# Optimization experiments

Hardware: AMD Instinct MI355X
Metric: run time of the kernel (lower is better)

Reference implementation:

```python
import jax, jax.numpy as jnp
import numpy as np

HEAD_DIM = 64
NUM_LANDMARKS = 64
SEQ_LEN = 4096
N_ITER = 6


def setup_inputs() -> dict:
    key = jax.random.key(0)
    kq, kk, kv = jax.random.split(key, 3)
    shape = (4, 12, SEQ_LEN, HEAD_DIM)  # [B, H, S, D]
    return {
        "Q": jax.random.normal(kq, shape, dtype=jnp.float32),
        "K": jax.random.normal(kk, shape, dtype=jnp.float32),
        "V": jax.random.normal(kv, shape, dtype=jnp.float32),
    }


def iterative_inv(mat, n_iter=N_ITER):
    # Newton-Schulz iteration for Moore-Penrose pseudo-inverse.
    L = mat.shape[-1]
    I = jnp.eye(L, dtype=mat.dtype)
    Km = mat
    # global (over all batch/head) max of row/col L1 norms
    scale = 1.0 / (jnp.max(jnp.sum(jnp.abs(Km), axis=-2)) * jnp.max(jnp.sum(jnp.abs(Km), axis=-1)))
    Vm = scale * jnp.swapaxes(Km, -1, -2)
    for _ in range(n_iter):
        KV = jnp.matmul(Km, Vm)
        Vm = jnp.matmul(0.25 * Vm, 13.0 * I - jnp.matmul(KV, 15.0 * I - jnp.matmul(KV, 7.0 * I - KV)))
    return Vm


def reference(Q, K, V):
    B, H, S, D = Q.shape
    m = NUM_LANDMARKS
    inv_scale = 1.0 / np.sqrt(np.sqrt(HEAD_DIM))
    Q = Q * inv_scale
    K = K * inv_scale
    # landmark pooling: mean over segments of length S // m
    Q_land = Q.reshape(B, H, m, S // m, D).mean(axis=-2)  # [B,H,m,D]
    K_land = K.reshape(B, H, m, S // m, D).mean(axis=-2)  # [B,H,m,D]
    kernel_1 = jax.nn.softmax(jnp.einsum("bhsd,bhmd->bhsm", Q, K_land), axis=-1)      # [B,H,S,m]
    kernel_2 = jax.nn.softmax(jnp.einsum("bhmd,bhnd->bhmn", Q_land, K_land), axis=-1)  # [B,H,m,m]
    kernel_3 = jax.nn.softmax(jnp.einsum("bhmd,bhsd->bhms", Q_land, K), axis=-1)       # [B,H,m,S]
    X = jnp.matmul(jnp.matmul(kernel_1, iterative_inv(kernel_2)), jnp.matmul(kernel_3, V))
    return X
```

## Files before the change

kernel.cpp:

```cpp
#include <hip/hip_runtime.h>
#include <cstdint>

#define BH 48
#define SEQ 4096
#define DIM 64
#define SEG 64
#define NCHUNK 8
#define CHUNK 512
#define PAD 68
#define BSTR 72

static constexpr float INV_SCALE = 0.35355339059327379f;

#define OFF_QL   0u
#define OFF_KL   196608u
#define OFF_K2   393216u
#define OFF_W    589824u
#define OFF_P    786432u
#define OFF_MNUM 983040u
#define OFF_MDEN 2555904u
#define OFF_CMAX 2580480u
#define OFF_RMAX 2580528u

typedef __attribute__((ext_vector_type(8))) short short8;
typedef __attribute__((ext_vector_type(4))) float f32x4;
#define MFMA16(a,b,c) __builtin_amdgcn_mfma_f32_16x16x32_bf16(a,b,c,0,0,0)

__device__ __forceinline__ float4 ld4(const float* p){ return *reinterpret_cast<const float4*>(p); }
__device__ __forceinline__ void st4(float* p, float4 v){ *reinterpret_cast<float4*>(p) = v; }

__device__ __forceinline__ unsigned short bfh_(float x){
  unsigned u = __float_as_uint(x);
  return (unsigned short)((u + 0x7fffu + ((u>>16)&1u)) >> 16);
}
__device__ __forceinline__ unsigned short bfl_(float x, unsigned short h){
  float r = x - __uint_as_float(((unsigned)h)<<16);
  return (unsigned short)(__float_as_uint(r) >> 16);
}
__device__ __forceinline__ void split4(float4 v, uint2& hi, uint2& lo){
  unsigned short h0=bfh_(v.x), h1=bfh_(v.y), h2=bfh_(v.z), h3=bfh_(v.w);
  unsigned short l0=bfl_(v.x,h0), l1=bfl_(v.y,h1), l2=bfl_(v.z,h2), l3=bfl_(v.w,h3);
  hi = make_uint2((unsigned)h0 | ((unsigned)h1<<16), (unsigned)h2 | ((unsigned)h3<<16));
  lo = make_uint2((unsigned)l0 | ((unsigned)l1<<16), (unsigned)l2 | ((unsigned)l3<<16));
}
__device__ __forceinline__ short8 mk8(uint2 a, uint2 b){
  union { short8 s; uint4 u; } x; x.u = make_uint4(a.x,a.y,b.x,b.y); return x.s;
}

__device__ __forceinline__ void mm_tile(float c[4][4], const float (*A)[PAD], const float (*B)[PAD], int i0, int j0){
  #pragma unroll 4
  for(int k=0;k<64;k+=4){
    float4 a4[4];
    #pragma unroll
    for(int r=0;r<4;r++) a4[r] = ld4(&A[i0+r][k]);
    #pragma unroll
    for(int kk=0;kk<4;kk++){
      float4 bv = ld4(&B[k+kk][j0]);
      #pragma unroll
      for(int r=0;r<4;r++){
        float a = ((const float*)&a4[r])[kk];
        c[r][0] += a*bv.x; c[r][1] += a*bv.y; c[r][2] += a*bv.z; c[r][3] += a*bv.w;
      }
    }
  }
}

__device__ __forceinline__ void mm_tile_gA(float c[4][4], const float* __restrict__ gA, const float (*B)[PAD], int i0, int j0){
  #pragma unroll 4
  for(int k=0;k<64;k+=4){
    float4 a4[4];
    #pragma unroll
    for(int r=0;r<4;r++) a4[r] = ld4(gA + (i0+r)*64 + k);
    #pragma unroll
    for(int kk=0;kk<4;kk++){
      float4 bv = ld4(&B[k+kk][j0]);
      #pragma unroll
      for(int r=0;r<4;r++){
        float a = ((const float*)&a4[r])[kk];
        c[r][0] += a*bv.x; c[r][1] += a*bv.y; c[r][2] += a*bv.z; c[r][3] += a*bv.w;
      }
    }
  }
}

__device__ __forceinline__ void mm_tile_diag(float c[4][4], const float (*A)[PAD], const float (*B)[PAD], int i0, int j0, float dg){
  #pragma unroll 4
  for(int k=0;k<64;k+=4){
    float4 a4[4];
    #pragma unroll
    for(int r=0;r<4;r++) a4[r] = ld4(&A[i0+r][k]);
    #pragma unroll
    for(int kk=0;kk<4;kk++){
      float4 bv = ld4(&B[k+kk][j0]);
      float b0=-bv.x, b1=-bv.y, b2=-bv.z, b3=-bv.w;
      int dd = k+kk-j0;
      if(dd==0) b0+=dg; else if(dd==1) b1+=dg; else if(dd==2) b2+=dg; else if(dd==3) b3+=dg;
      #pragma unroll
      for(int r=0;r<4;r++){
        float a = ((const float*)&a4[r])[kk];
        c[r][0]+=a*b0; c[r][1]+=a*b1; c[r][2]+=a*b2; c[r][3]+=a*b3;
      }
    }
  }
}

__global__ __launch_bounds__(256) void pool_kernel(const float* __restrict__ Qg, const float* __restrict__ Kg, float* __restrict__ ws){
  int bx = blockIdx.x;
  int head = bx >> 5;
  int rest = bx & 31;
  int tensor = rest >> 4;
  int l0 = (rest & 15) * 4;
  int t = threadIdx.x;
  int ll = t >> 6;
  int lane = t & 63;
  int d4 = (lane & 15) * 4;
  int rq = lane >> 4;
  const float* src = tensor ? Kg : Qg;
  float* dst = ws + (tensor ? OFF_KL : OFF_QL);
  int l = l0 + ll;
  const float* base = src + ((size_t)head*SEQ + (size_t)l*SEG)*DIM + d4;
  float sx=0.f, sy=0.f, sz=0.f, sw=0.f;
  #pragma unroll 4
  for(int r=rq; r<SEG; r+=4){
    float4 v = ld4(base + (size_t)r*DIM);
    sx+=v.x; sy+=v.y; sz+=v.z; sw+=v.w;
  }
  sx += __shfl_xor(sx,16); sy += __shfl_xor(sy,16); sz += __shfl_xor(sz,16); sw += __shfl_xor(sw,16);
  sx += __shfl_xor(sx,32); sy += __shfl_xor(sy,32); sz += __shfl_xor(sz,32); sw += __shfl_xor(sw,32);
  if(rq==0){
    const float sc = INV_SCALE / 64.0f;
    float4 o; o.x=sx*sc; o.y=sy*sc; o.z=sz*sc; o.w=sw*sc;
    st4(dst + ((size_t)head*64 + l)*DIM + d4, o);
  }
}

__global__ __launch_bounds__(256) void k2_kernel(float* __restrict__ ws){
  __shared__ float sQ[64][65];
  __shared__ float sK[64][65];
  __shared__ float sE[64][65];
  __shared__ float red[128];
  int h = blockIdx.x, t = threadIdx.x;
  const float* QL = ws + OFF_QL + (size_t)h*4096;
  const float* KL = ws + OFF_KL + (size_t)h*4096;
  for(int i=t;i<4096;i+=256){ sQ[i>>6][i&63]=QL[i]; sK[i>>6][i&63]=KL[i]; }
  __syncthreads();
  int i = t>>2, q = t&3;
  float l[16];
  #pragma unroll
  for(int jj=0;jj<16;jj++){
    int j = q*16+jj;
    float s=0.f;
    for(int d=0;d<64;d++) s += sQ[i][d]*sK[j][d];
    l[jj]=s;
  }
  float mx = l[0];
  #pragma unroll
  for(int jj=1;jj<16;jj++) mx = fmaxf(mx,l[jj]);
  mx = fmaxf(mx, __shfl_xor(mx,1));
  mx = fmaxf(mx, __shfl_xor(mx,2));
  float sum=0.f;
  #pragma unroll
  for(int jj=0;jj<16;jj++){ l[jj]=__expf(l[jj]-mx); sum+=l[jj]; }
  sum += __shfl_xor(sum,1);
  sum += __shfl_xor(sum,2);
  float inv = 1.0f/sum;
  #pragma unroll
  for(int jj=0;jj<16;jj++) sE[i][q*16+jj] = l[jj]*inv;
  __syncthreads();
  float* K2 = ws + OFF_K2 + (size_t)h*4096;
  for(int idx=t; idx<4096; idx+=256) K2[idx] = sE[idx>>6][idx&63];
  if(t<64){
    float cs=0.f, rs=0.f;
    for(int r=0;r<64;r++){ cs += sE[r][t]; rs += sE[t][r]; }
    red[t]=cs; red[64+t]=rs;
  }
  __syncthreads();
  if(t==0){
    float cm=0.f, rm=0.f;
    for(int j=0;j<64;j++){ cm=fmaxf(cm,red[j]); rm=fmaxf(rm,red[64+j]); }
    ws[OFF_CMAX+h]=cm; ws[OFF_RMAX+h]=rm;
  }
}

__global__ __launch_bounds__(256) void fused_kernel(const float* __restrict__ Kg, const float* __restrict__ Vg, float* __restrict__ ws){
  __shared__ __align__(16) unsigned char smem[74752];
  __shared__ float sscale;
  int bid = blockIdx.x, t = threadIdx.x;
  const int lane=t&63, w=t>>6, ln=lane&15, g=lane>>4;
  const int rr=t>>4, c4=(t&15)*4;
  if(bid < BH){
    int h = bid;
    const float* K2 = ws + OFF_K2 + (size_t)h*4096;
    unsigned short* Uh=(unsigned short*)smem;
    unsigned short* Ul=Uh+4608;
    unsigned short* Rh=Uh+9216;
    unsigned short* Rl=Uh+13824;
    unsigned short* Ch=Uh+18432;
    unsigned short* Cl=Uh+23040;
    unsigned short* Gh=Uh+27648;
    unsigned short* Gl=Uh+32256;
    short8 kmh[2],kml[2];
    #pragma unroll
    for(int kh=0;kh<2;kh++){
      const float* p=K2+(16*w+ln)*64+32*kh+8*g;
      float4 x0=ld4(p), x1=ld4(p+4);
      uint2 h0,l0,h1,l1; split4(x0,h0,l0); split4(x1,h1,l1);
      kmh[kh]=mk8(h0,h1); kml[kh]=mk8(l0,l1);
    }
    if(t<64){
      float cm=(lane<BH)?ws[OFF_CMAX+lane]:0.f;
      float rm=(lane<BH)?ws[OFF_RMAX+lane]:0.f;
      #pragma unroll
      for(int s=32;s>=1;s>>=1){ cm=fmaxf(cm,__shfl_xor(cm,s)); rm=fmaxf(rm,__shfl_xor(rm,s)); }
      if(t==0) sscale=1.0f/(cm*rm);
    }
    __syncthreads();
    float scale=sscale;
    #pragma unroll
    for(int gg=0;gg<4;gg++){
      int m=rr+16*gg;
      float4 v=ld4(K2+m*64+c4);
      v.x*=scale; v.y*=scale; v.z*=scale; v.w*=scale;
      uint2 hi,lo; split4(v,hi,lo);
      *reinterpret_cast<uint2*>(Uh+m*BSTR+c4)=hi;
      *reinterpret_cast<uint2*>(Ul+m*BSTR+c4)=lo;
      float fv[4]={v.x,v.y,v.z,v.w};
      #pragma unroll
      for(int e=0;e<4;e++){
        unsigned short hv=bfh_(fv[e]);
        Rh[(c4+e)*BSTR+m]=hv;
        Rl[(c4+e)*BSTR+m]=bfl_(fv[e],hv);
      }
    }
    __syncthreads();
    f32x4 dA[4];
    short8 ah[2],al[2];
    for(int it=0; it<5; it++){
      #pragma unroll
      for(int ni=0;ni<4;ni++){
        f32x4 d=(f32x4){0.f,0.f,0.f,0.f};
        #pragma unroll
        for(int kh=0;kh<2;kh++){
          int bb=(16*ni+ln)*BSTR+32*kh+8*g;
          short8 bh=*reinterpret_cast<const short8*>(Uh+bb);
          short8 bl=*reinterpret_cast<const short8*>(Ul+bb);
          d=MFMA16(kmh[kh],bh,d); d=MFMA16(kmh[kh],bl,d); d=MFMA16(kml[kh],bh,d);
        }
        dA[ni]=d;
      }
      #pragma unroll
      for(int ni=0;ni<4;ni++){
        int j=16*ni+ln;
        float4 tv; float* pv=(float*)&tv;
        #pragma unroll
        for(int r=0;r<4;r++){
          float v=dA[ni][r];
          int i=16*w+4*g+r;
          unsigned short hv=bfh_(v);
          Ch[i*BSTR+j]=hv; Cl[i*BSTR+j]=bfl_(v,hv);
          pv[r]=((i==j)?7.0f:0.0f)-v;
        }
        uint2 hi,lo; split4(tv,hi,lo);
        *reinterpret_cast<uint2*>(Gh+j*BSTR+16*w+4*g)=hi;
        *reinterpret_cast<uint2*>(Gl+j*BSTR+16*w+4*g)=lo;
      }
      __syncthreads();
      #pragma unroll
      for(int kh=0;kh<2;kh++){
        int ab=(16*w+ln)*BSTR+32*kh+8*g;
        ah[kh]=*reinterpret_cast<const short8*>(Ch+ab);
        al[kh]=*reinterpret_cast<const short8*>(Cl+ab);
      }
      #pragma unroll
      for(int ni=0;ni<4;ni++){
        f32x4 d=(f32x4){0.f,0.f,0.f,0.f};
        #pragma unroll
        for(int kh=0;kh<2;kh++){
          int bb=(16*ni+ln)*BSTR+32*kh+8*g;
          short8 bh=*reinterpret_cast<const short8*>(Gh+bb);
          short8 bl=*reinterpret_cast<const short8*>(Gl+bb);
          d=MFMA16(ah[kh],bh,d); d=MFMA16(ah[kh],bl,d); d=MFMA16(al[kh],bh,d);
        }
        dA[ni]=d;
      }
      __syncthreads();
      #pragma unroll
      for(int ni=0;ni<4;ni++){
        int j=16*ni+ln;
        float4 tv; float* pv=(float*)&tv;
        #pragma unroll
        for(int r=0;r<4;r++){ int i=16*w+4*g+r; pv[r]=((i==j)?15.0f:0.0f)-dA[ni][r]; }
        uint2 hi,lo; split4(tv,hi,lo);
        *reinterpret_cast<uint2*>(Gh+j*BSTR+16*w+4*g)=hi;
        *reinterpret_cast<uint2*>(Gl+j*BSTR+16*w+4*g)=lo;
      }
      __syncthreads();
      #pragma unroll
      for(int ni=0;ni<4;ni++){
        f32x4 d=(f32x4){0.f,0.f,0.f,0.f};
        #pragma unroll
        for(int kh=0;kh<2;kh++){
          int bb=(16*ni+ln)*BSTR+32*kh+8*g;
          short8 bh=*reinterpret_cast<const short8*>(Gh+bb);
          short8 bl=*reinterpret_cast<const short8*>(Gl+bb);
          d=MFMA16(ah[kh],bh,d); d=MFMA16(ah[kh],bl,d); d=MFMA16(al[kh],bh,d);
        }
        dA[ni]=d;
      }
      __syncthreads();
      #pragma unroll
      for(int ni=0;ni<4;ni++){
        int j=16*ni+ln;
        float4 tv; float* pv=(float*)&tv;
        #pragma unroll
        for(int r=0;r<4;r++){ int i=16*w+4*g+r; pv[r]=((i==j)?13.0f:0.0f)-dA[ni][r]; }
        uint2 hi,lo; split4(tv,hi,lo);
        *reinterpret_cast<uint2*>(Ch+j*BSTR+16*w+4*g)=hi;
        *reinterpret_cast<uint2*>(Cl+j*BSTR+16*w+4*g)=lo;
      }
      __syncthreads();
      #pragma unroll
      for(int kh=0;kh<2;kh++){
        int ab=(16*w+ln)*BSTR+32*kh+8*g;
        ah[kh]=*reinterpret_cast<const short8*>(Rh+ab);
        al[kh]=*reinterpret_cast<const short8*>(Rl+ab);
      }
      #pragma unroll
      for(int ni=0;ni<4;ni++){
        f32x4 d=(f32x4){0.f,0.f,0.f,0.f};
        #pragma unroll
        for(int kh=0;kh<2;kh++){
          int bb=(16*ni+ln)*BSTR+32*kh+8*g;
          short8 bh=*reinterpret_cast<const short8*>(Ch+bb);
          short8 bl=*reinterpret_cast<const short8*>(Cl+bb);
          d=MFMA16(ah[kh],bh,d); d=MFMA16(ah[kh],bl,d); d=MFMA16(al[kh],bh,d);
        }
        dA[ni]=d;
      }
      __syncthreads();
      #pragma unroll
      for(int ni=0;ni<4;ni++){
        int j=16*ni+ln;
        float4 tv; float* pv=(float*)&tv;
        #pragma unroll
        for(int r=0;r<4;r++){
          float v=0.25f*dA[ni][r];
          int i=16*w+4*g+r;
          unsigned short hv=bfh_(v);
          Rh[i*BSTR+j]=hv; Rl[i*BSTR+j]=bfl_(v,hv);
          pv[r]=v;
        }
        uint2 hi,lo; split4(tv,hi,lo);
        *reinterpret_cast<uint2*>(Uh+j*BSTR+16*w+4*g)=hi;
        *reinterpret_cast<uint2*>(Ul+j*BSTR+16*w+4*g)=lo;
      }
      __syncthreads();
    }
    float (*Vmf)[PAD]=(float(*)[PAD])(smem+36864);
    for(int i=t;i<4096;i+=256){
      int r_=i>>6, c_=i&63;
      float v=__uint_as_float(((unsigned)Rh[r_*BSTR+c_])<<16)
             +__uint_as_float(((unsigned)Rl[r_*BSTR+c_])<<16);
      Vmf[r_][c_]=v;
    }
    __syncthreads();
    float (*B1)[PAD]=(float(*)[PAD])(smem);
    float (*B2)[PAD]=(float(*)[PAD])(smem+17408);
    int i0=(t>>4)*4, j0=(t&15)*4;
    {
      float c[4][4]={};
      mm_tile_gA(c,K2,Vmf,i0,j0);
      #pragma unroll
      for(int r=0;r<4;r++){ float4 o; o.x=c[r][0];o.y=c[r][1];o.z=c[r][2];o.w=c[r][3]; st4(&B1[i0+r][j0],o); }
      __syncthreads();
    }
    {
      float c[4][4]={};
      mm_tile_diag(c,B1,B1,i0,j0,7.0f);
      #pragma unroll
      for(int r=0;r<4;r++){ float4 o; o.x=c[r][0];o.y=c[r][1];o.z=c[r][2];o.w=c[r][3]; st4(&B2[i0+r][j0],o); }
      __syncthreads();
    }
    {
      float c[4][4]={};
      mm_tile_diag(c,B1,B2,i0,j0,15.0f);
      __syncthreads();
      #pragma unroll
      for(int r=0;r<4;r++){ float4 o; o.x=c[r][0];o.y=c[r][1];o.z=c[r][2];o.w=c[r][3]; st4(&B1[i0+r][j0],o); }
      __syncthreads();
    }
    {
      float c[4][4]={};
      mm_tile_diag(c,Vmf,B1,i0,j0,13.0f);
      __syncthreads();
      #pragma unroll
      for(int r=0;r<4;r++){ float4 o; o.x=0.25f*c[r][0];o.y=0.25f*c[r][1];o.z=0.25f*c[r][2];o.w=0.25f*c[r][3]; st4(&Vmf[i0+r][j0],o); }
      __syncthreads();
    }
    float* W = ws + OFF_W + (size_t)h*4096;
    for(int i=t;i<4096;i+=256) W[i] = Vmf[i>>6][i&63];
  } else {
    int b = bid - BH;
    int h = b >> 3, ch = b & 7;
    unsigned short* QLh=(unsigned short*)smem;
    unsigned short* QLl=QLh+4608;
    unsigned short* Kth=QLh+9216;
    unsigned short* Ktl=QLh+13824;
    unsigned short* VTh=QLh+18432;
    unsigned short* VTl=QLh+23040;
    unsigned short* PTh=QLh+27648;
    unsigned short* PTl=QLh+32256;
    float* sden=(float*)(smem+73728);
    const float* QL = ws + OFF_QL + (size_t)h*4096;
    #pragma unroll
    for(int gg=0;gg<4;gg++){
      int m=rr+16*gg;
      float4 v=ld4(QL+m*64+c4);
      uint2 hi,lo; split4(v,hi,lo);
      *reinterpret_cast<uint2*>(QLh+m*BSTR+c4)=hi;
      *reinterpret_cast<uint2*>(QLl+m*BSTR+c4)=lo;
    }
    const size_t kbase=((size_t)h*SEQ+(size_t)ch*CHUNK)*DIM;
    float4 kr[4],vr[4];
    #pragma unroll
    for(int gg=0;gg<4;gg++){
      size_t off=kbase+(size_t)(rr+16*gg)*DIM+c4;
      kr[gg]=ld4(Kg+off); vr[gg]=ld4(Vg+off);
    }
    f32x4 acc[4];
    #pragma unroll
    for(int ni=0;ni<4;ni++) acc[ni]=(f32x4){0.f,0.f,0.f,0.f};
    float den_acc[4]={0.f,0.f,0.f,0.f};
    for(int tile=0;tile<8;tile++){
      __syncthreads();
      #pragma unroll
      for(int gg=0;gg<4;gg++){
        int r=rr+16*gg;
        float4 kv=kr[gg];
        kv.x*=INV_SCALE; kv.y*=INV_SCALE; kv.z*=INV_SCALE; kv.w*=INV_SCALE;
        uint2 hi,lo; split4(kv,hi,lo);
        *reinterpret_cast<uint2*>(Kth+r*BSTR+c4)=hi;
        *reinterpret_cast<uint2*>(Ktl+r*BSTR+c4)=lo;
        float fv[4]={vr[gg].x,vr[gg].y,vr[gg].z,vr[gg].w};
        #pragma unroll
        for(int e=0;e<4;e++){
          int d=c4+e;
          unsigned short hv=bfh_(fv[e]);
          unsigned short lv=bfl_(fv[e],hv);
          int sp = r ^ (((d>>2)&7)<<3);
          VTh[d*BSTR+sp]=hv; VTl[d*BSTR+sp]=lv;
        }
      }
      if(tile<7){
        #pragma unroll
        for(int gg=0;gg<4;gg++){
          size_t off=kbase+(size_t)((tile+1)*64+rr+16*gg)*DIM+c4;
          kr[gg]=ld4(Kg+off); vr[gg]=ld4(Vg+off);
        }
      }
      __syncthreads();
      short8 kah[2],kal[2];
      #pragma unroll
      for(int kh=0;kh<2;kh++){
        int ab=(16*w+ln)*BSTR+32*kh+8*g;
        kah[kh]=*reinterpret_cast<const short8*>(Kth+ab);
        kal[kh]=*reinterpret_cast<const short8*>(Ktl+ab);
      }
      #pragma unroll
      for(int ni=0;ni<4;ni++){
        f32x4 dl=(f32x4){0.f,0.f,0.f,0.f};
        #pragma unroll
        for(int kh=0;kh<2;kh++){
          int bb=(16*ni+ln)*BSTR+32*kh+8*g;
          short8 bh=*reinterpret_cast<const short8*>(QLh+bb);
          short8 bl=*reinterpret_cast<const short8*>(QLl+bb);
          dl=MFMA16(kah[kh],bh,dl);
          dl=MFMA16(kah[kh],bl,dl);
          dl=MFMA16(kal[kh],bh,dl);
        }
        float p0=__expf(dl[0]), p1=__expf(dl[1]), p2=__expf(dl[2]), p3=__expf(dl[3]);
        den_acc[ni]+=p0+p1+p2+p3;
        unsigned short h0=bfh_(p0),h1=bfh_(p1),h2=bfh_(p2),h3=bfh_(p3);
        unsigned short l0=bfl_(p0,h0),l1=bfl_(p1,h1),l2=bfl_(p2,h2),l3=bfl_(p3,h3);
        int pb=(16*ni+ln)*BSTR+16*w+4*g;
        *reinterpret_cast<uint2*>(PTh+pb)=make_uint2((unsigned)h0|((unsigned)h1<<16),(unsigned)h2|((unsigned)h3<<16));
        *reinterpret_cast<uint2*>(PTl+pb)=make_uint2((unsigned)l0|((unsigned)l1<<16),(unsigned)l2|((unsigned)l3<<16));
      }
      __syncthreads();
      short8 pah[2],pal[2];
      #pragma unroll
      for(int kh=0;kh<2;kh++){
        int pb=(16*w+ln)*BSTR+32*kh+8*g;
        pah[kh]=*reinterpret_cast<const short8*>(PTh+pb);
        pal[kh]=*reinterpret_cast<const short8*>(PTl+pb);
      }
      #pragma unroll
      for(int ni=0;ni<4;ni++){
        int row=16*ni+ln;
        int swz=((row>>2)&7)<<3;
        #pragma unroll
        for(int kh=0;kh<2;kh++){
          int vb=row*BSTR+((32*kh+8*g)^swz);
          short8 vh=*reinterpret_cast<const short8*>(VTh+vb);
          short8 vl=*reinterpret_cast<const short8*>(VTl+vb);
          acc[ni]=MFMA16(pah[kh],vh,acc[ni]);
          acc[ni]=MFMA16(pah[kh],vl,acc[ni]);
          acc[ni]=MFMA16(pal[kh],vh,acc[ni]);
        }
      }
    }
    float* num = ws + OFF_MNUM + (size_t)b*4096;
    #pragma unroll
    for(int ni=0;ni<4;ni++){
      #pragma unroll
      for(int r=0;r<4;r++) num[(16*w+4*g+r)*64+16*ni+ln]=acc[ni][r];
      den_acc[ni]+=__shfl_xor(den_acc[ni],16);
      den_acc[ni]+=__shfl_xor(den_acc[ni],32);
    }
    if(lane<16){
      #pragma unroll
      for(int ni=0;ni<4;ni++) sden[w*64+16*ni+lane]=den_acc[ni];
    }
    __syncthreads();
    if(t<64) ws[OFF_MDEN+(size_t)b*64+t]=sden[t]+sden[64+t]+sden[128+t]+sden[192+t];
  }
}

__global__ __launch_bounds__(256) void combine_kernel(float* __restrict__ ws){
  __shared__ float sW[64][PAD];
  __shared__ float sM[64][PAD];
  __shared__ float sden[64];
  int h=blockIdx.x, t=threadIdx.x;
  if(t<64){
    float s=0.f;
    for(int c=0;c<NCHUNK;c++) s += ws[OFF_MDEN + ((size_t)h*NCHUNK+c)*64 + t];
    sden[t]=1.0f/s;
  }
  for(int i=t;i<4096;i+=256) sW[i>>6][i&63] = ws[OFF_W + (size_t)h*4096 + i];
  __syncthreads();
  for(int i=t;i<1024;i+=256){
    int m=i>>4, d4=(i&15)*4;
    float sx=0.f,sy=0.f,sz=0.f,sw2=0.f;
    for(int c=0;c<NCHUNK;c++){
      float4 v = ld4(ws + OFF_MNUM + ((size_t)h*NCHUNK+c)*4096 + m*64 + d4);
      sx+=v.x; sy+=v.y; sz+=v.z; sw2+=v.w;
    }
    float iv = sden[m];
    float4 o; o.x=sx*iv; o.y=sy*iv; o.z=sz*iv; o.w=sw2*iv;
    st4(&sM[m][d4], o);
  }
  __syncthreads();
  int i0=(t>>4)*4, j0=(t&15)*4;
  float c[4][4]={};
  mm_tile(c, sW, sM, i0, j0);
  float* P = ws + OFF_P + (size_t)h*4096;
  #pragma unroll
  for(int r=0;r<4;r++){
    float4 o; o.x=c[r][0]; o.y=c[r][1]; o.z=c[r][2]; o.w=c[r][3];
    st4(P + (i0+r)*64 + j0, o);
  }
}

__global__ __launch_bounds__(256) void final_kernel(const float* __restrict__ Qg, float* __restrict__ out, const float* __restrict__ ws){
  __shared__ float sKLT[64][PAD];
  __shared__ float sP[64][PAD];
  __shared__ float sQE[64][PAD];
  int bid=blockIdx.x, t=threadIdx.x;
  int h=bid>>6, s0=(bid&63)*64;
  const float* KL = ws + OFF_KL + (size_t)h*4096;
  const float* P  = ws + OFF_P  + (size_t)h*4096;
  const float* Qb = Qg + ((size_t)h*SEQ + (size_t)s0)*DIM;
  for(int i=t;i<1024;i+=256){
    int m=i>>4, d4=(i&15)*4;
    float4 v = ld4(KL + m*64 + d4);
    sKLT[d4+0][m]=v.x; sKLT[d4+1][m]=v.y; sKLT[d4+2][m]=v.z; sKLT[d4+3][m]=v.w;
    st4(&sP[m][d4], ld4(P + m*64 + d4));
    float4 q = ld4(Qb + (size_t)m*DIM + d4);
    q.x*=INV_SCALE; q.y*=INV_SCALE; q.z*=INV_SCALE; q.w*=INV_SCALE;
    st4(&sQE[m][d4], q);
  }
  __syncthreads();
  int i0=(t>>4)*4, j0=(t&15)*4;
  float l[4][4]={};
  mm_tile(l, sQE, sKLT, i0, j0);
  float e[4][4]; float rs[4];
  #pragma unroll
  for(int r=0;r<4;r++){
    float s=0.f;
    #pragma unroll
    for(int cc=0;cc<4;cc++){ e[r][cc]=__expf(l[r][cc]); s+=e[r][cc]; }
    rs[r]=s;
  }
  #pragma unroll
  for(int r=0;r<4;r++){
    rs[r]+=__shfl_xor(rs[r],1);
    rs[r]+=__shfl_xor(rs[r],2);
    rs[r]+=__shfl_xor(rs[r],4);
    rs[r]+=__shfl_xor(rs[r],8);
  }
  __syncthreads();
  #pragma unroll
  for(int r=0;r<4;r++){ float4 o; o.x=e[r][0]; o.y=e[r][1]; o.z=e[r][2]; o.w=e[r][3]; st4(&sQE[i0+r][j0], o); }
  __syncthreads();
  float c[4][4]={};
  mm_tile(c, sQE, sP, i0, j0);
  #pragma unroll
  for(int r=0;r<4;r++){
    float iv = 1.0f/rs[r];
    float4 o; o.x=c[r][0]*iv; o.y=c[r][1]*iv; o.z=c[r][2]*iv; o.w=c[r][3]*iv;
    st4(out + ((size_t)h*SEQ + (size_t)(s0+i0+r))*DIM + j0, o);
  }
}

extern "C" void kernel_launch(void* const* d_in, const int* in_sizes, int n_in,
                              void* d_out, int out_size, void* d_ws, size_t ws_size,
                              hipStream_t stream) {
  const float* Q = (const float*)d_in[0];
  const float* K = (const float*)d_in[1];
  const float* V = (const float*)d_in[2];
  float* out = (float*)d_out;
  float* ws  = (float*)d_ws;

  pool_kernel   <<<BH*32, 256, 0, stream>>>(Q, K, ws);
  k2_kernel     <<<BH,    256, 0, stream>>>(ws);
  fused_kernel  <<<BH + BH*NCHUNK, 256, 0, stream>>>(K, V, ws);
  combine_kernel<<<BH,    256, 0, stream>>>(ws);
  final_kernel  <<<BH*64, 256, 0, stream>>>(Q, out, ws);
}
```

Baseline: 269.7 us.

## Use split-bf16 MFMA for final landmark softmax and P matmuls

Rewrites final_kernel so both 64x64x64 products (Q·K_land^T and softmax·P) run on bf16 MFMA instructions, using a hi/lo split with three MFMAs to keep near-fp32 accuracy, in place of scalar FP32 register tiling. Operands are staged in LDS as bf16 hi/lo planes, and the buffers are reused for the transposed P and the exp tile. Row sums are reduced through shuffles plus a small LDS array. This trades extra packing work and a precision risk from the bf16x3 approximation for higher matrix throughput. Output stores become scalar rather than float4, which may reduce store coalescing.

```diff
diff --git a/kernel.cpp b/kernel.cpp
--- a/kernel.cpp
+++ b/kernel.cpp
@@ -562,53 +562,110 @@
 }
 
 __global__ __launch_bounds__(256) void final_kernel(const float* __restrict__ Qg, float* __restrict__ out, const float* __restrict__ ws){
-  __shared__ float sKLT[64][PAD];
-  __shared__ float sP[64][PAD];
-  __shared__ float sQE[64][PAD];
+  __shared__ __align__(16) unsigned char smem[37888];
   int bid=blockIdx.x, t=threadIdx.x;
   int h=bid>>6, s0=(bid&63)*64;
+  const int lane=t&63, w=t>>6, ln=lane&15, g=lane>>4;
+  const int rr=t>>4, c4=(t&15)*4;
+  unsigned short* QBh=(unsigned short*)smem;
+  unsigned short* QBl=QBh+4608;
+  unsigned short* KLh=QBh+9216;
+  unsigned short* KLl=QBh+13824;
+  float* sdenw=(float*)(smem+36864);
   const float* KL = ws + OFF_KL + (size_t)h*4096;
   const float* P  = ws + OFF_P  + (size_t)h*4096;
   const float* Qb = Qg + ((size_t)h*SEQ + (size_t)s0)*DIM;
-  for(int i=t;i<1024;i+=256){
-    int m=i>>4, d4=(i&15)*4;
-    float4 v = ld4(KL + m*64 + d4);
-    sKLT[d4+0][m]=v.x; sKLT[d4+1][m]=v.y; sKLT[d4+2][m]=v.z; sKLT[d4+3][m]=v.w;
-    st4(&sP[m][d4], ld4(P + m*64 + d4));
-    float4 q = ld4(Qb + (size_t)m*DIM + d4);
+  float4 p2r[4];
+  #pragma unroll
+  for(int gg=0;gg<4;gg++){
+    int row=rr+16*gg;
+    p2r[gg]=ld4(P+row*64+c4);
+    float4 q=ld4(Qb+(size_t)row*DIM+c4);
     q.x*=INV_SCALE; q.y*=INV_SCALE; q.z*=INV_SCALE; q.w*=INV_SCALE;
-    st4(&sQE[m][d4], q);
-  }
-  __syncthreads();
-  int i0=(t>>4)*4, j0=(t&15)*4;
-  float l[4][4]={};
-  mm_tile(l, sQE, sKLT, i0, j0);
-  float e[4][4]; float rs[4];
+    uint2 hi,lo; split4(q,hi,lo);
+    *reinterpret_cast<uint2*>(QBh+row*BSTR+c4)=hi;
+    *reinterpret_cast<uint2*>(QBl+row*BSTR+c4)=lo;
+    float4 kl=ld4(KL+row*64+c4);
+    split4(kl,hi,lo);
+    *reinterpret_cast<uint2*>(KLh+row*BSTR+c4)=hi;
+    *reinterpret_cast<uint2*>(KLl+row*BSTR+c4)=lo;
+  }
+  __syncthreads();
+  short8 ah_[2],al_[2];
+  #pragma unroll
+  for(int kh=0;kh<2;kh++){
+    int ab=(16*w+ln)*BSTR+32*kh+8*g;
+    ah_[kh]=*reinterpret_cast<const short8*>(KLh+ab);
+    al_[kh]=*reinterpret_cast<const short8*>(KLl+ab);
+  }
+  f32x4 dl[4];
+  #pragma unroll
+  for(int ni=0;ni<4;ni++){
+    f32x4 d=(f32x4){0.f,0.f,0.f,0.f};
+    #pragma unroll
+    for(int kh=0;kh<2;kh++){
+      int bb=(16*ni+ln)*BSTR+32*kh+8*g;
+      short8 bh=*reinterpret_cast<const short8*>(QBh+bb);
+      short8 bl=*reinterpret_cast<const short8*>(QBl+bb);
+      d=MFMA16(ah_[kh],bh,d); d=MFMA16(ah_[kh],bl,d); d=MFMA16(al_[kh],bh,d);
+    }
+    dl[ni]=d;
+  }
+  __syncthreads();
+  #pragma unroll
+  for(int gg=0;gg<4;gg++){
+    int row=rr+16*gg;
+    float fp[4]={p2r[gg].x,p2r[gg].y,p2r[gg].z,p2r[gg].w};
+    #pragma unroll
+    for(int e=0;e<4;e++){
+      unsigned short hv=bfh_(fp[e]);
+      QBh[(c4+e)*BSTR+row]=hv;
+      QBl[(c4+e)*BSTR+row]=bfl_(fp[e],hv);
+    }
+  }
+  float den_acc[4];
+  #pragma unroll
+  for(int ni=0;ni<4;ni++){
+    float p0=__expf(dl[ni][0]), p1=__expf(dl[ni][1]), p2v=__expf(dl[ni][2]), p3v=__expf(dl[ni][3]);
+    den_acc[ni]=p0+p1+p2v+p3v;
+    unsigned short h0=bfh_(p0),h1=bfh_(p1),h2=bfh_(p2v),h3=bfh_(p3v);
+    unsigned short e0=bfl_(p0,h0),e1=bfl_(p1,h1),e2=bfl_(p2v,h2),e3=bfl_(p3v,h3);
+    int pb=(16*ni+ln)*BSTR+16*w+4*g;
+    *reinterpret_cast<uint2*>(KLh+pb)=make_uint2((unsigned)h0|((unsigned)h1<<16),(unsigned)h2|((unsigned)h3<<16));
+    *reinterpret_cast<uint2*>(KLl+pb)=make_uint2((unsigned)e0|((unsigned)e1<<16),(unsigned)e2|((unsigned)e3<<16));
+    den_acc[ni]+=__shfl_xor(den_acc[ni],16);
+    den_acc[ni]+=__shfl_xor(den_acc[ni],32);
+  }
+  if(lane<16){
+    #pragma unroll
+    for(int ni=0;ni<4;ni++) sdenw[w*64+16*ni+lane]=den_acc[ni];
+  }
+  __syncthreads();
+  #pragma unroll
+  for(int kh=0;kh<2;kh++){
+    int ab=(16*w+ln)*BSTR+32*kh+8*g;
+    ah_[kh]=*reinterpret_cast<const short8*>(KLh+ab);
+    al_[kh]=*reinterpret_cast<const short8*>(KLl+ab);
+  }
+  float inv[4];
   #pragma unroll
   for(int r=0;r<4;r++){
-    float s=0.f;
-    #pragma unroll
-    for(int cc=0;cc<4;cc++){ e[r][cc]=__expf(l[r][cc]); s+=e[r][cc]; }
-    rs[r]=s;
-  }
-  #pragma unroll
-  for(int r=0;r<4;r++){
-    rs[r]+=__shfl_xor(rs[r],1);
-    rs[r]+=__shfl_xor(rs[r],2);
-    rs[r]+=__shfl_xor(rs[r],4);
-    rs[r]+=__shfl_xor(rs[r],8);
-  }
-  __syncthreads();
-  #pragma unroll
-  for(int r=0;r<4;r++){ float4 o; o.x=e[r][0]; o.y=e[r][1]; o.z=e[r][2]; o.w=e[r][3]; st4(&sQE[i0+r][j0], o); }
-  __syncthreads();
-  float c[4][4]={};
-  mm_tile(c, sQE, sP, i0, j0);
-  #pragma unroll
-  for(int r=0;r<4;r++){
-    float iv = 1.0f/rs[r];
-    float4 o; o.x=c[r][0]*iv; o.y=c[r][1]*iv; o.z=c[r][2]*iv; o.w=c[r][3]*iv;
-    st4(out + ((size_t)h*SEQ + (size_t)(s0+i0+r))*DIM + j0, o);
+    int s=16*w+4*g+r;
+    inv[r]=1.0f/(sdenw[s]+sdenw[64+s]+sdenw[128+s]+sdenw[192+s]);
+  }
+  #pragma unroll
+  for(int ni=0;ni<4;ni++){
+    f32x4 d=(f32x4){0.f,0.f,0.f,0.f};
+    #pragma unroll
+    for(int kh=0;kh<2;kh++){
+      int bb=(16*ni+ln)*BSTR+32*kh+8*g;
+      short8 bh=*reinterpret_cast<const short8*>(QBh+bb);
+      short8 bl=*reinterpret_cast<const short8*>(QBl+bb);
+      d=MFMA16(ah_[kh],bh,d); d=MFMA16(ah_[kh],bl,d); d=MFMA16(al_[kh],bh,d);
+    }
+    #pragma unroll
+    for(int r=0;r<4;r++)
+      out[((size_t)h*SEQ + (size_t)(s0+16*w+4*g+r))*DIM + 16*ni+ln] = d[r]*inv[r];
   }
 }
 
```

Result: faster. 244.1 us (-9.5%).
